# Kernel optimization log

Measured on AMD Instinct MI355X. Metric: run time of the kernel, lower is better.

The kernel has to match this reference:

```python
import jax, jax.numpy as jnp
import numpy as np
from jax import lax

B, S, V, E, H, T = 128, 512, 30000, 256, 256, 9
PAD_ID = 0


def setup_inputs() -> dict:
    key = jax.random.key(0)
    ks = jax.random.split(key, 16)
    u = lambda k, sh, s: jax.random.uniform(k, sh, jnp.float32, -s, s)
    sc = 1.0 / float(np.sqrt(H))
    so = 1.0 / float(np.sqrt(2 * H))
    input_ids = jax.random.randint(ks[0], (B, S), 1, V)
    lengths = jax.random.randint(ks[1], (B,), 1, S + 1)
    mask = jnp.arange(S)[None, :] < lengths[:, None]  # left-contiguous valid mask
    embed_table = jax.random.normal(ks[2], (V, E), jnp.float32).at[PAD_ID].set(0.0)
    return dict(
        input_ids=input_ids,
        mask=mask,
        embed_table=embed_table,
        W_ih_f=u(ks[3], (4 * H, E), sc), W_hh_f=u(ks[4], (4 * H, H), sc), b_f=u(ks[5], (4 * H,), sc),
        W_ih_b=u(ks[6], (4 * H, E), sc), W_hh_b=u(ks[7], (4 * H, H), sc), b_b=u(ks[8], (4 * H,), sc),
        W_out=u(ks[9], (T, 2 * H), so), b_out=u(ks[10], (T,), so),
        start_trans=u(ks[11], (T,), 0.1), end_trans=u(ks[12], (T,), 0.1), trans=u(ks[13], (T, T), 0.1),
    )


def _lstm_dir(xg, W_hh, reverse):
    # xg: [S, B, 4H] precomputed input projection + bias; torch gate order i,f,g,o
    def step(carry, g_in):
        h, c = carry
        g = g_in + h @ W_hh.T
        i, f, gg, o = jnp.split(g, 4, axis=-1)
        c = jax.nn.sigmoid(f) * c + jax.nn.sigmoid(i) * jnp.tanh(gg)
        h = jax.nn.sigmoid(o) * jnp.tanh(c)
        return (h, c), h
    b, hdim = xg.shape[1], W_hh.shape[1]
    init = (jnp.zeros((b, hdim), xg.dtype), jnp.zeros((b, hdim), xg.dtype))
    _, hs = lax.scan(step, init, xg, reverse=reverse)
    return hs  # [S, B, H]


def _emissions(input_ids, embed_table, W_ih_f, W_hh_f, b_f, W_ih_b, W_hh_b, b_b, W_out, b_out):
    x = embed_table[input_ids]                                  # [B, S, E]
    xg_f = jnp.einsum('bse,ge->sbg', x, W_ih_f) + b_f           # [S, B, 4H]
    xg_b = jnp.einsum('bse,ge->sbg', x, W_ih_b) + b_b
    h_f = _lstm_dir(xg_f, W_hh_f, reverse=False)
    h_b = _lstm_dir(xg_b, W_hh_b, reverse=True)
    h = jnp.concatenate([h_f, h_b], axis=-1)                    # [S, B, 2H]
    return jnp.einsum('sbh,th->sbt', h, W_out) + b_out          # [S, B, T]


def reference(input_ids, mask, embed_table, W_ih_f, W_hh_f, b_f, W_ih_b, W_hh_b, b_b,
              W_out, b_out, start_trans, end_trans, trans):
    em = _emissions(input_ids, embed_table, W_ih_f, W_hh_f, b_f, W_ih_b, W_hh_b, b_b, W_out, b_out)
    maskT = mask.T  # [S, B]

    # ---- Viterbi forward (torchcrf._viterbi_decode semantics) ----
    score0 = start_trans + em[0]  # [B, T]

    def vstep(score, inp):
        em_t, m_t = inp  # [B,T], [B]
        nxt = score[:, :, None] + trans[None, :, :] + em_t[:, None, :]  # [B, T, T]
        idx = jnp.argmax(nxt, axis=1)        # [B, T] backpointers
        best = jnp.max(nxt, axis=1)          # [B, T]
        score = jnp.where(m_t[:, None], best, score)
        return score, idx

    score, history = lax.scan(vstep, score0, (em[1:], maskT[1:]))  # history: [S-1, B, T]
    last_tag = jnp.argmax(score + end_trans, axis=-1)              # [B]

    # ---- Backtrace (mask-aware; frontier stays put on padded steps) ----
    def btstep(tag, inp):
        hist_t, m_t = inp  # [B,T], [B]
        out = tag
        prev = jnp.take_along_axis(hist_t, tag[:, None], axis=1)[:, 0]
        tag = jnp.where(m_t, prev, tag)
        return tag, out

    tag0, tags_rest = lax.scan(btstep, last_tag, (history, maskT[1:]), reverse=True)
    tags = jnp.concatenate([tag0[None, :], tags_rest], axis=0).T  # [B, S]
    return jnp.where(mask, tags, 0).astype(jnp.int32)
```

## Files before the change

### kernel.cpp

```cpp
#include <hip/hip_runtime.h>
#include <hip/hip_bf16.h>

#define SEQ   512
#define BATCH 128
#define VOCAB 30000
#define EDIM  256
#define HDIM  256
#define NT    9

__global__ void k_detect(const unsigned char* __restrict__ m, int* __restrict__ flag) {
    __shared__ int ok_sh;
    if (threadIdx.x == 0) ok_sh = 1;
    __syncthreads();
    int b = threadIdx.x;
    const uint4* row = (const uint4*)(m + b * SEQ);
    int ok = 1, prev = 1;
    for (int i = 0; i < SEQ / 16; ++i) {
        uint4 v = row[i];
        unsigned w[4] = {v.x, v.y, v.z, v.w};
        #pragma unroll
        for (int wi = 0; wi < 4; ++wi) {
            #pragma unroll
            for (int j = 0; j < 4; ++j) {
                int byte = (w[wi] >> (8 * j)) & 255;
                if (byte > 1 || byte > prev) ok = 0;
                prev = byte;
            }
        }
    }
    if (!ok) atomicAnd(&ok_sh, 0);
    __syncthreads();
    if (threadIdx.x == 0) *flag = ok_sh;
}

__global__ __launch_bounds__(256) void k_table_gemm(
    const float* __restrict__ emb, const float* __restrict__ Wf,
    const float* __restrict__ Wb, const float* __restrict__ bf,
    const float* __restrict__ bb, float* __restrict__ table) {
    __shared__ __align__(16) float As[64][68];
    __shared__ __align__(16) float Bs[64][68];
    int t  = threadIdx.x;
    int tx = t & 15, ty = t >> 4;
    int n0 = blockIdx.x * 64;
    int v0 = blockIdx.y * 64;
    float acc[4][4] = {};
    for (int kc = 0; kc < 4; ++kc) {
        #pragma unroll
        for (int rr = 0; rr < 4; ++rr) {
            int slot = t + rr * 256;
            int m = slot >> 4, kq = slot & 15;
            int v = v0 + m;
            float4 a = (v < VOCAB)
                ? *(const float4*)&emb[v * EDIM + kc * 64 + kq * 4]
                : make_float4(0.f, 0.f, 0.f, 0.f);
            As[kq * 4 + 0][m] = a.x; As[kq * 4 + 1][m] = a.y;
            As[kq * 4 + 2][m] = a.z; As[kq * 4 + 3][m] = a.w;
            int n = n0 + m;
            const float* Wrow = (n < 1024) ? &Wf[n * 256] : &Wb[(n - 1024) * 256];
            float4 bvec = *(const float4*)&Wrow[kc * 64 + kq * 4];
            Bs[kq * 4 + 0][m] = bvec.x; Bs[kq * 4 + 1][m] = bvec.y;
            Bs[kq * 4 + 2][m] = bvec.z; Bs[kq * 4 + 3][m] = bvec.w;
        }
        __syncthreads();
        #pragma unroll
        for (int k = 0; k < 64; ++k) {
            float4 a = *(const float4*)&As[k][ty * 4];
            float4 b = *(const float4*)&Bs[k][tx * 4];
            acc[0][0] += a.x * b.x; acc[0][1] += a.x * b.y; acc[0][2] += a.x * b.z; acc[0][3] += a.x * b.w;
            acc[1][0] += a.y * b.x; acc[1][1] += a.y * b.y; acc[1][2] += a.y * b.z; acc[1][3] += a.y * b.w;
            acc[2][0] += a.z * b.x; acc[2][1] += a.z * b.y; acc[2][2] += a.z * b.z; acc[2][3] += a.z * b.w;
            acc[3][0] += a.w * b.x; acc[3][1] += a.w * b.y; acc[3][2] += a.w * b.z; acc[3][3] += a.w * b.w;
        }
        __syncthreads();
    }
    int n = n0 + tx * 4;
    const float* bi = (n < 1024) ? &bf[n] : &bb[n - 1024];
    float4 bias = *(const float4*)bi;
    #pragma unroll
    for (int i = 0; i < 4; ++i) {
        int v = v0 + ty * 4 + i;
        if (v < VOCAB) {
            float4 o;
            o.x = acc[i][0] + bias.x; o.y = acc[i][1] + bias.y;
            o.z = acc[i][2] + bias.z; o.w = acc[i][3] + bias.w;
            *(float4*)&table[(size_t)v * 2048 + n] = o;
        }
    }
}

#define DPPXOR(dst, src, CTRL) { \
    int _i = __float_as_int(src); \
    int _r = __builtin_amdgcn_update_dpp(_i, _i, (CTRL), 0xF, 0xF, false); \
    dst = __int_as_float(_r); }

__global__ __attribute__((amdgpu_flat_work_group_size(512, 512), amdgpu_waves_per_eu(2, 2)))
void k_lstm_cl(
    const int* __restrict__ ids, const float* __restrict__ Whhf,
    const float* __restrict__ Whhb, const float* __restrict__ table,
    const float* __restrict__ Wout, float* __restrict__ emp,
    float* hx, int* tagbuf) {
    __shared__ float h_cur[8][256];
    __shared__ float h_em[256];
    __shared__ float sh_g[8][132];
    __shared__ float wout_s[NT][257];
    __shared__ int   sh_ctr;

    const int t   = threadIdx.x;
    const int bid = blockIdx.x;
    const int cluster = bid >> 3;
    const int myb = bid & 7;
    const int dir = cluster & 1;
    const int oct = cluster >> 1;
    const int gbatch = oct * 8 + myb;

    const int lane = t & 63;
    const int wv   = t >> 6;
    const int g    = t >> 4;
    const int kc   = t & 15;

    const int nb = t >> 5, nd = t & 31;
    const int em = t - 256;
    const int etg = em >> 4, el = em & 15;

    const float* Whh = dir ? Whhb : Whhf;

    if (t == 0) sh_ctr = 0;
    for (int idx = t; idx < NT * 256; idx += 512)
        wout_s[idx >> 8][idx & 255] = Wout[(idx >> 8) * 512 + dir * 256 + (idx & 255)];
    for (int idx = t; idx < 2048; idx += 512)
        h_cur[idx >> 8][idx & 255] = 0.f;
    float c_state = 0.f;

    float4 w0_0, w0_1, w0_2, w0_3, w1_0, w1_1, w1_2, w1_3;
    float4 w2_0, w2_1, w2_2, w2_3, w3_0, w3_1, w3_2, w3_3;
    {
        int lr0 = 4 * g, lr1 = 4 * g + 1, lr2 = 4 * g + 2, lr3 = 4 * g + 3;
        int gr0 = (lr0 >> 5) * 256 + myb * 32 + (lr0 & 31);
        int gr1 = (lr1 >> 5) * 256 + myb * 32 + (lr1 & 31);
        int gr2 = (lr2 >> 5) * 256 + myb * 32 + (lr2 & 31);
        int gr3 = (lr3 >> 5) * 256 + myb * 32 + (lr3 & 31);
        const float4* wp0 = (const float4*)(Whh + (size_t)gr0 * 256);
        const float4* wp1 = (const float4*)(Whh + (size_t)gr1 * 256);
        const float4* wp2 = (const float4*)(Whh + (size_t)gr2 * 256);
        const float4* wp3 = (const float4*)(Whh + (size_t)gr3 * 256);
        w0_0 = wp0[kc]; w0_1 = wp0[kc + 16]; w0_2 = wp0[kc + 32]; w0_3 = wp0[kc + 48];
        w1_0 = wp1[kc]; w1_1 = wp1[kc + 16]; w1_2 = wp1[kc + 32]; w1_3 = wp1[kc + 48];
        w2_0 = wp2[kc]; w2_1 = wp2[kc + 16]; w2_2 = wp2[kc + 32]; w2_3 = wp2[kc + 48];
        w3_0 = wp3[kc]; w3_1 = wp3[kc + 16]; w3_2 = wp3[kc + 32]; w3_3 = wp3[kc + 48];
    }
    __syncthreads();

    float xi = 0.f, xf = 0.f, xq = 0.f, xo = 0.f;
    if (t < 256) {
        int s0 = dir ? SEQ - 1 : 0;
        int id = ids[(oct * 8 + nb) * SEQ + s0];
        const float* tb = table + (size_t)id * 2048 + dir * 1024;
        int base = myb * 32 + nd;
        xi = tb[base]; xf = tb[256 + base]; xq = tb[512 + base]; xo = tb[768 + base];
    }

    #pragma unroll 1
    for (int it = 0; it < SEQ; ++it) {
        if (t < 256) h_em[t] = h_cur[myb][t];

        float a[32];
        #pragma unroll
        for (int m = 0; m < 32; ++m) a[m] = 0.f;

        #define DOTJ(J, W0, W1, W2, W3) { \
            const int off = 4 * (kc + 16 * (J)); \
            _Pragma("unroll") \
            for (int b = 0; b < 8; ++b) { \
                float4 hv = *(const float4*)(&h_cur[b][0] + off); \
                a[b]      += W0.x*hv.x + W0.y*hv.y + W0.z*hv.z + W0.w*hv.w; \
                a[8 + b]  += W1.x*hv.x + W1.y*hv.y + W1.z*hv.z + W1.w*hv.w; \
                a[16 + b] += W2.x*hv.x + W2.y*hv.y + W2.z*hv.z + W2.w*hv.w; \
                a[24 + b] += W3.x*hv.x + W3.y*hv.y + W3.z*hv.z + W3.w*hv.w; } }
        DOTJ(0, w0_0, w1_0, w2_0, w3_0)
        DOTJ(1, w0_1, w1_1, w2_1, w3_1)
        DOTJ(2, w0_2, w1_2, w2_2, w3_2)
        DOTJ(3, w0_3, w1_3, w2_3, w3_3)
        #undef DOTJ

        #pragma unroll
        for (int m = 0; m < 16; ++m) {
            int bit = kc & 1;
            float sent = bit ? a[m] : a[m + 16];
            float recv; DPPXOR(recv, sent, 0xB1)
            a[m] = (bit ? a[m + 16] : a[m]) + recv;
        }
        #pragma unroll
        for (int m = 0; m < 8; ++m) {
            int bit = kc & 2;
            float sent = bit ? a[m] : a[m + 8];
            float recv; DPPXOR(recv, sent, 0x4E)
            a[m] = (bit ? a[m + 8] : a[m]) + recv;
        }
        #pragma unroll
        for (int m = 0; m < 4; ++m) {
            int bit = kc & 4;
            float sent = bit ? a[m] : a[m + 4];
            float recv = __shfl_xor(sent, 4);
            a[m] = (bit ? a[m + 4] : a[m]) + recv;
        }
        #pragma unroll
        for (int m = 0; m < 2; ++m) {
            int bit = kc & 8;
            float sent = bit ? a[m] : a[m + 2];
            float recv; DPPXOR(recv, sent, 0x128)
            a[m] = (bit ? a[m + 2] : a[m]) + recv;
        }
        {
            int m0 = ((kc & 1) << 4) | ((kc & 2) << 2) | (kc & 4) | ((kc & 8) >> 2);
            int r = m0 >> 3, b = m0 & 7;
            sh_g[b][4 * g + r] = a[0];
            sh_g[b + 1][4 * g + r] = a[1];
        }
        __syncthreads();

        const int p = it & 1;
        float* hxp = hx + (size_t)p * 65536 + (size_t)cluster * 2048;
        int* tags = tagbuf + p * 256 + cluster * 8;

        if (t < 256) {
            float iv = sh_g[nb][nd]      + xi;
            float fv = sh_g[nb][32 + nd] + xf;
            float gv = sh_g[nb][64 + nd] + xq;
            float ov = sh_g[nb][96 + nd] + xo;
            float si = 1.f / (1.f + expf(-iv));
            float sf = 1.f / (1.f + expf(-fv));
            float so = 1.f / (1.f + expf(-ov));
            float tg = tanhf(gv);
            c_state = sf * c_state + si * tg;
            float hh = so * tanhf(c_state);
            int dl = myb * 32 + nd;
            h_cur[nb][dl] = hh;
            __hip_atomic_store(&hxp[nb * 256 + dl], hh,
                               __ATOMIC_RELAXED, __HIP_MEMORY_SCOPE_AGENT);
            asm volatile("s_waitcnt vmcnt(0)" ::: "memory");
            if (lane == 0) atomicAdd(&sh_ctr, 1);
            if (t == 0) {
                while (__hip_atomic_load(&sh_ctr, __ATOMIC_RELAXED,
                                         __HIP_MEMORY_SCOPE_WORKGROUP) < 4 * (it + 1)) {}
                __hip_atomic_store(&tags[myb], it,
                                   __ATOMIC_RELAXED, __HIP_MEMORY_SCOPE_AGENT);
            }
            if (it < SEQ - 1) {
                int sn = dir ? (SEQ - 2 - it) : (it + 1);
                int id = ids[(oct * 8 + nb) * SEQ + sn];
                const float* tb = table + (size_t)id * 2048 + dir * 1024;
                int base = myb * 32 + nd;
                xi = tb[base]; xf = tb[256 + base]; xq = tb[512 + base]; xo = tb[768 + base];
            }
        } else if (em < 144) {
            if (it > 0) {
                int sp = dir ? (SEQ - it) : (it - 1);
                float pe = 0.f;
                #pragma unroll
                for (int j = 0; j < 16; ++j)
                    pe += wout_s[etg][el + 16 * j] * h_em[el + 16 * j];
                pe += __shfl_xor(pe, 1); pe += __shfl_xor(pe, 2);
                pe += __shfl_xor(pe, 4); pe += __shfl_xor(pe, 8);
                if (el == 0)
                    emp[(((size_t)(dir * BATCH) + gbatch) * SEQ + sp) * NT + etg] = pe;
            }
        }

        if (wv != myb) {
            while (__hip_atomic_load(&tags[wv], __ATOMIC_RELAXED,
                                     __HIP_MEMORY_SCOPE_AGENT) != it)
                __builtin_amdgcn_s_sleep(1);
            #pragma unroll
            for (int rep = 0; rep < 4; ++rep) {
                int idx = rep * 64 + lane;
                int nb2 = idx >> 5, nd2 = idx & 31;
                float vv = __hip_atomic_load(&hxp[nb2 * 256 + wv * 32 + nd2],
                                             __ATOMIC_RELAXED, __HIP_MEMORY_SCOPE_AGENT);
                h_cur[nb2][wv * 32 + nd2] = vv;
            }
        }
        __syncthreads();
    }

    if (t < 256) h_em[t] = h_cur[myb][t];
    __syncthreads();
    if (t < 144) {
        int etg2 = t >> 4, el2 = t & 15;
        int sp = dir ? 0 : (SEQ - 1);
        float pe = 0.f;
        #pragma unroll
        for (int j = 0; j < 16; ++j)
            pe += wout_s[etg2][el2 + 16 * j] * h_em[el2 + 16 * j];
        pe += __shfl_xor(pe, 1); pe += __shfl_xor(pe, 2);
        pe += __shfl_xor(pe, 4); pe += __shfl_xor(pe, 8);
        if (el2 == 0)
            emp[(((size_t)(dir * BATCH) + gbatch) * SEQ + sp) * NT + etg2] = pe;
    }
}

__global__ __launch_bounds__(64) void k_viterbi(
    const float* __restrict__ emp, const float* __restrict__ b_out,
    const float* __restrict__ start_t, const float* __restrict__ end_t,
    const float* __restrict__ trans, const void* __restrict__ maskp,
    const int* __restrict__ mask_is_bool, int* __restrict__ out) {
    __shared__ float sh_em[SEQ][NT];
    __shared__ float sh_score[NT];
    __shared__ float sh_trans[NT * NT];
    __shared__ unsigned char sh_mask[SEQ];
    __shared__ unsigned char sh_hist[SEQ - 1][NT];
    __shared__ unsigned char sh_tags[SEQ];
    int b = blockIdx.x;
    int t = threadIdx.x;
    int isb = *mask_is_bool;
    for (int idx = t; idx < SEQ * NT; idx += 64) {
        int s = idx / NT, tg = idx % NT;
        sh_em[s][tg] = emp[((size_t)b * SEQ + s) * NT + tg]
                     + emp[(((size_t)BATCH + b) * SEQ + s) * NT + tg]
                     + b_out[tg];
    }
    if (isb) {
        const unsigned char* m8 = (const unsigned char*)maskp;
        for (int idx = t; idx < SEQ; idx += 64) sh_mask[idx] = m8[b * SEQ + idx];
    } else {
        const int* m32 = (const int*)maskp;
        for (int idx = t; idx < SEQ; idx += 64) sh_mask[idx] = (unsigned char)(m32[b * SEQ + idx] != 0);
    }
    for (int idx = t; idx < NT * NT; idx += 64) sh_trans[idx] = trans[idx];
    __syncthreads();
    float sc = 0.f;
    if (t < NT) { sc = start_t[t] + sh_em[0][t]; sh_score[t] = sc; }
    __syncthreads();
    for (int s = 1; s < SEQ; ++s) {
        if (t < NT) {
            float m = -3.4e38f; int bp = 0;
            #pragma unroll
            for (int i = 0; i < NT; ++i) {
                float v = sh_score[i] + sh_trans[i * NT + t];
                if (v > m) { m = v; bp = i; }
            }
            sh_hist[s - 1][t] = (unsigned char)bp;
            float best = m + sh_em[s][t];
            if (sh_mask[s]) sc = best;
        }
        __syncthreads();
        if (t < NT) sh_score[t] = sc;
        __syncthreads();
    }
    if (t == 0) {
        float bb = -3.4e38f; int tag = 0;
        for (int j = 0; j < NT; ++j) {
            float v = sh_score[j] + end_t[j];
            if (v > bb) { bb = v; tag = j; }
        }
        for (int pos = SEQ - 1; pos >= 1; --pos) {
            sh_tags[pos] = (unsigned char)tag;
            if (sh_mask[pos]) tag = sh_hist[pos - 1][tag];
        }
        sh_tags[0] = (unsigned char)tag;
    }
    __syncthreads();
    for (int idx = t; idx < SEQ; idx += 64) {
        out[b * SEQ + idx] = sh_mask[idx] ? (int)sh_tags[idx] : 0;
    }
}

extern "C" void kernel_launch(void* const* d_in, const int* in_sizes, int n_in,
                              void* d_out, int out_size, void* d_ws, size_t ws_size,
                              hipStream_t stream) {
    const int*   ids  = (const int*)d_in[0];
    const void*  mask = d_in[1];
    const float* emb  = (const float*)d_in[2];
    const float* Wihf = (const float*)d_in[3];
    const float* Whhf = (const float*)d_in[4];
    const float* bfv  = (const float*)d_in[5];
    const float* Wihb = (const float*)d_in[6];
    const float* Whhb = (const float*)d_in[7];
    const float* bbv  = (const float*)d_in[8];
    const float* Wout = (const float*)d_in[9];
    const float* bout = (const float*)d_in[10];
    const float* st   = (const float*)d_in[11];
    const float* en   = (const float*)d_in[12];
    const float* tr   = (const float*)d_in[13];
    int* out = (int*)d_out;

    char* ws = (char*)d_ws;
    float* table = (float*)ws;
    float* emp   = (float*)(ws + 245760000);
    float* hx    = (float*)(ws + 245760000 + 4718592);
    int*   tags  = (int*)(ws + 245760000 + 4718592 + 524288);
    int*   flag  = (int*)(ws + 245760000 + 4718592 + 524288 + 2048);

    k_detect<<<1, 128, 0, stream>>>((const unsigned char*)mask, flag);
    dim3 g1(32, 469);
    k_table_gemm<<<g1, 256, 0, stream>>>(emb, Wihf, Wihb, bfv, bbv, table);
    k_lstm_cl<<<256, 512, 0, stream>>>(ids, Whhf, Whhb, table, Wout, emp, hx, tags);
    k_viterbi<<<128, 64, 0, stream>>>(emp, bout, st, en, tr, mask, flag, out);
}
```

Before: 3.861 ms.

## Halve batch per LSTM cluster and double block count to spread recurrence work

Each 8-block cluster of the persistent LSTM kernel now handles 4 batch rows instead of 8, and the grid grows from 256 to 512 blocks. Per-step dot products, the DPP reductions, gate math and the global hidden-state exchange all shrink by half per block. Occupancy is raised to 4 waves per EU so two blocks can share a CU. The aim is a shorter per-timestep critical path in this latency-bound recurrence. The cost is twice as many spin-synchronized blocks that must all be co-resident, a tighter register budget, and two blocks competing for each CU.

```diff
diff --git a/kernel.cpp b/kernel.cpp
--- a/kernel.cpp
+++ b/kernel.cpp
@@ -93,32 +93,34 @@
     int _r = __builtin_amdgcn_update_dpp(_i, _i, (CTRL), 0xF, 0xF, false); \
     dst = __int_as_float(_r); }
 
-__global__ __attribute__((amdgpu_flat_work_group_size(512, 512), amdgpu_waves_per_eu(2, 2)))
+__global__ __attribute__((amdgpu_flat_work_group_size(512, 512), amdgpu_waves_per_eu(4, 4)))
 void k_lstm_cl(
     const int* __restrict__ ids, const float* __restrict__ Whhf,
     const float* __restrict__ Whhb, const float* __restrict__ table,
     const float* __restrict__ Wout, float* __restrict__ emp,
     float* hx, int* tagbuf) {
-    __shared__ float h_cur[8][256];
+    __shared__ float h_cur[4][256];
     __shared__ float h_em[256];
-    __shared__ float sh_g[8][132];
+    __shared__ float sh_g[4][132];
     __shared__ float wout_s[NT][257];
     __shared__ int   sh_ctr;
 
     const int t   = threadIdx.x;
     const int bid = blockIdx.x;
     const int cluster = bid >> 3;
-    const int myb = bid & 7;
+    const int myd = bid & 7;
     const int dir = cluster & 1;
-    const int oct = cluster >> 1;
-    const int gbatch = oct * 8 + myb;
+    const int quad = cluster >> 1;
+    const int gbatch = quad * 4 + myd;
 
     const int lane = t & 63;
     const int wv   = t >> 6;
     const int g    = t >> 4;
     const int kc   = t & 15;
 
-    const int nb = t >> 5, nd = t & 31;
+    const int nb = (t >> 5) & 3;
+    const int nd = t & 31;
+
     const int em = t - 256;
     const int etg = em >> 4, el = em & 15;
 
@@ -127,7 +129,7 @@
     if (t == 0) sh_ctr = 0;
     for (int idx = t; idx < NT * 256; idx += 512)
         wout_s[idx >> 8][idx & 255] = Wout[(idx >> 8) * 512 + dir * 256 + (idx & 255)];
-    for (int idx = t; idx < 2048; idx += 512)
+    for (int idx = t; idx < 1024; idx += 512)
         h_cur[idx >> 8][idx & 255] = 0.f;
     float c_state = 0.f;
 
@@ -135,10 +137,10 @@
     float4 w2_0, w2_1, w2_2, w2_3, w3_0, w3_1, w3_2, w3_3;
     {
         int lr0 = 4 * g, lr1 = 4 * g + 1, lr2 = 4 * g + 2, lr3 = 4 * g + 3;
-        int gr0 = (lr0 >> 5) * 256 + myb * 32 + (lr0 & 31);
-        int gr1 = (lr1 >> 5) * 256 + myb * 32 + (lr1 & 31);
-        int gr2 = (lr2 >> 5) * 256 + myb * 32 + (lr2 & 31);
-        int gr3 = (lr3 >> 5) * 256 + myb * 32 + (lr3 & 31);
+        int gr0 = (lr0 >> 5) * 256 + myd * 32 + (lr0 & 31);
+        int gr1 = (lr1 >> 5) * 256 + myd * 32 + (lr1 & 31);
+        int gr2 = (lr2 >> 5) * 256 + myd * 32 + (lr2 & 31);
+        int gr3 = (lr3 >> 5) * 256 + myd * 32 + (lr3 & 31);
         const float4* wp0 = (const float4*)(Whh + (size_t)gr0 * 256);
         const float4* wp1 = (const float4*)(Whh + (size_t)gr1 * 256);
         const float4* wp2 = (const float4*)(Whh + (size_t)gr2 * 256);
@@ -151,31 +153,31 @@
     __syncthreads();
 
     float xi = 0.f, xf = 0.f, xq = 0.f, xo = 0.f;
-    if (t < 256) {
+    if (t < 128) {
         int s0 = dir ? SEQ - 1 : 0;
-        int id = ids[(oct * 8 + nb) * SEQ + s0];
+        int id = ids[(quad * 4 + nb) * SEQ + s0];
         const float* tb = table + (size_t)id * 2048 + dir * 1024;
-        int base = myb * 32 + nd;
+        int base = myd * 32 + nd;
         xi = tb[base]; xf = tb[256 + base]; xq = tb[512 + base]; xo = tb[768 + base];
     }
 
     #pragma unroll 1
     for (int it = 0; it < SEQ; ++it) {
-        if (t < 256) h_em[t] = h_cur[myb][t];
-
-        float a[32];
-        #pragma unroll
-        for (int m = 0; m < 32; ++m) a[m] = 0.f;
+        if (myd < 4 && t < 256) h_em[t] = h_cur[myd][t];
+
+        float a[16];
+        #pragma unroll
+        for (int m = 0; m < 16; ++m) a[m] = 0.f;
 
         #define DOTJ(J, W0, W1, W2, W3) { \
             const int off = 4 * (kc + 16 * (J)); \
             _Pragma("unroll") \
-            for (int b = 0; b < 8; ++b) { \
+            for (int b = 0; b < 4; ++b) { \
                 float4 hv = *(const float4*)(&h_cur[b][0] + off); \
                 a[b]      += W0.x*hv.x + W0.y*hv.y + W0.z*hv.z + W0.w*hv.w; \
-                a[8 + b]  += W1.x*hv.x + W1.y*hv.y + W1.z*hv.z + W1.w*hv.w; \
-                a[16 + b] += W2.x*hv.x + W2.y*hv.y + W2.z*hv.z + W2.w*hv.w; \
-                a[24 + b] += W3.x*hv.x + W3.y*hv.y + W3.z*hv.z + W3.w*hv.w; } }
+                a[4 + b]  += W1.x*hv.x + W1.y*hv.y + W1.z*hv.z + W1.w*hv.w; \
+                a[8 + b]  += W2.x*hv.x + W2.y*hv.y + W2.z*hv.z + W2.w*hv.w; \
+                a[12 + b] += W3.x*hv.x + W3.y*hv.y + W3.z*hv.z + W3.w*hv.w; } }
         DOTJ(0, w0_0, w1_0, w2_0, w3_0)
         DOTJ(1, w0_1, w1_1, w2_1, w3_1)
         DOTJ(2, w0_2, w1_2, w2_2, w3_2)
@@ -183,46 +185,43 @@
         #undef DOTJ
 
         #pragma unroll
-        for (int m = 0; m < 16; ++m) {
+        for (int m = 0; m < 8; ++m) {
             int bit = kc & 1;
-            float sent = bit ? a[m] : a[m + 16];
+            float sent = bit ? a[m] : a[m + 8];
             float recv; DPPXOR(recv, sent, 0xB1)
-            a[m] = (bit ? a[m + 16] : a[m]) + recv;
-        }
-        #pragma unroll
-        for (int m = 0; m < 8; ++m) {
+            a[m] = (bit ? a[m + 8] : a[m]) + recv;
+        }
+        #pragma unroll
+        for (int m = 0; m < 4; ++m) {
             int bit = kc & 2;
-            float sent = bit ? a[m] : a[m + 8];
+            float sent = bit ? a[m] : a[m + 4];
             float recv; DPPXOR(recv, sent, 0x4E)
-            a[m] = (bit ? a[m + 8] : a[m]) + recv;
-        }
-        #pragma unroll
-        for (int m = 0; m < 4; ++m) {
+            a[m] = (bit ? a[m + 4] : a[m]) + recv;
+        }
+        #pragma unroll
+        for (int m = 0; m < 2; ++m) {
             int bit = kc & 4;
-            float sent = bit ? a[m] : a[m + 4];
+            float sent = bit ? a[m] : a[m + 2];
             float recv = __shfl_xor(sent, 4);
-            a[m] = (bit ? a[m + 4] : a[m]) + recv;
-        }
-        #pragma unroll
-        for (int m = 0; m < 2; ++m) {
+            a[m] = (bit ? a[m + 2] : a[m]) + recv;
+        }
+        {
             int bit = kc & 8;
-            float sent = bit ? a[m] : a[m + 2];
+            float sent = bit ? a[0] : a[1];
             float recv; DPPXOR(recv, sent, 0x128)
-            a[m] = (bit ? a[m + 2] : a[m]) + recv;
+            a[0] = (bit ? a[1] : a[0]) + recv;
         }
         {
-            int m0 = ((kc & 1) << 4) | ((kc & 2) << 2) | (kc & 4) | ((kc & 8) >> 2);
-            int r = m0 >> 3, b = m0 & 7;
-            sh_g[b][4 * g + r] = a[0];
-            sh_g[b + 1][4 * g + r] = a[1];
+            int tile = ((kc & 1) << 3) | ((kc & 2) << 1) | ((kc & 4) >> 1) | ((kc & 8) >> 3);
+            sh_g[tile & 3][4 * g + (tile >> 2)] = a[0];
         }
         __syncthreads();
 
         const int p = it & 1;
-        float* hxp = hx + (size_t)p * 65536 + (size_t)cluster * 2048;
-        int* tags = tagbuf + p * 256 + cluster * 8;
-
-        if (t < 256) {
+        float* hxp = hx + (size_t)p * 65536 + (size_t)cluster * 1024;
+        int* tags = tagbuf + p * 512 + cluster * 8;
+
+        if (t < 128) {
             float iv = sh_g[nb][nd]      + xi;
             float fv = sh_g[nb][32 + nd] + xf;
             float gv = sh_g[nb][64 + nd] + xq;
@@ -233,7 +232,7 @@
             float tg = tanhf(gv);
             c_state = sf * c_state + si * tg;
             float hh = so * tanhf(c_state);
-            int dl = myb * 32 + nd;
+            int dl = myd * 32 + nd;
             h_cur[nb][dl] = hh;
             __hip_atomic_store(&hxp[nb * 256 + dl], hh,
                                __ATOMIC_RELAXED, __HIP_MEMORY_SCOPE_AGENT);
@@ -241,18 +240,18 @@
             if (lane == 0) atomicAdd(&sh_ctr, 1);
             if (t == 0) {
                 while (__hip_atomic_load(&sh_ctr, __ATOMIC_RELAXED,
-                                         __HIP_MEMORY_SCOPE_WORKGROUP) < 4 * (it + 1)) {}
-                __hip_atomic_store(&tags[myb], it,
+                                         __HIP_MEMORY_SCOPE_WORKGROUP) < 2 * (it + 1)) {}
+                __hip_atomic_store(&tags[myd], it,
                                    __ATOMIC_RELAXED, __HIP_MEMORY_SCOPE_AGENT);
             }
             if (it < SEQ - 1) {
                 int sn = dir ? (SEQ - 2 - it) : (it + 1);
-                int id = ids[(oct * 8 + nb) * SEQ + sn];
+                int id = ids[(quad * 4 + nb) * SEQ + sn];
                 const float* tb = table + (size_t)id * 2048 + dir * 1024;
-                int base = myb * 32 + nd;
+                int base = myd * 32 + nd;
                 xi = tb[base]; xf = tb[256 + base]; xq = tb[512 + base]; xo = tb[768 + base];
             }
-        } else if (em < 144) {
+        } else if (em >= 0 && em < 144 && myd < 4) {
             if (it > 0) {
                 int sp = dir ? (SEQ - it) : (it - 1);
                 float pe = 0.f;
@@ -266,25 +265,25 @@
             }
         }
 
-        if (wv != myb) {
+        if (wv != myd) {
             while (__hip_atomic_load(&tags[wv], __ATOMIC_RELAXED,
                                      __HIP_MEMORY_SCOPE_AGENT) != it)
                 __builtin_amdgcn_s_sleep(1);
             #pragma unroll
-            for (int rep = 0; rep < 4; ++rep) {
+            for (int rep = 0; rep < 2; ++rep) {
                 int idx = rep * 64 + lane;
-                int nb2 = idx >> 5, nd2 = idx & 31;
-                float vv = __hip_atomic_load(&hxp[nb2 * 256 + wv * 32 + nd2],
+                int b2 = idx >> 5, nd2 = idx & 31;
+                float vv = __hip_atomic_load(&hxp[b2 * 256 + wv * 32 + nd2],
                                              __ATOMIC_RELAXED, __HIP_MEMORY_SCOPE_AGENT);
-                h_cur[nb2][wv * 32 + nd2] = vv;
-            }
-        }
-        __syncthreads();
-    }
-
-    if (t < 256) h_em[t] = h_cur[myb][t];
-    __syncthreads();
-    if (t < 144) {
+                h_cur[b2][wv * 32 + nd2] = vv;
+            }
+        }
+        __syncthreads();
+    }
+
+    if (myd < 4 && t < 256) h_em[t] = h_cur[myd][t];
+    __syncthreads();
+    if (myd < 4 && t < 144) {
         int etg2 = t >> 4, el2 = t & 15;
         int sp = dir ? 0 : (SEQ - 1);
         float pe = 0.f;
@@ -388,11 +387,11 @@
     float* emp   = (float*)(ws + 245760000);
     float* hx    = (float*)(ws + 245760000 + 4718592);
     int*   tags  = (int*)(ws + 245760000 + 4718592 + 524288);
-    int*   flag  = (int*)(ws + 245760000 + 4718592 + 524288 + 2048);
+    int*   flag  = (int*)(ws + 245760000 + 4718592 + 524288 + 4096);
 
     k_detect<<<1, 128, 0, stream>>>((const unsigned char*)mask, flag);
     dim3 g1(32, 469);
     k_table_gemm<<<g1, 256, 0, stream>>>(emb, Wihf, Wihb, bfv, bbv, table);
-    k_lstm_cl<<<256, 512, 0, stream>>>(ids, Whhf, Whhb, table, Wout, emp, hx, tags);
+    k_lstm_cl<<<512, 512, 0, stream>>>(ids, Whhf, Whhb, table, Wout, emp, hx, tags);
     k_viterbi<<<128, 64, 0, stream>>>(emp, bout, st, en, tr, mask, flag, out);
 }
```

Result: faster. 3.422 ms (-11.4%).
